# Kernel tuning notes

Hardware: AMD Instinct MI355X
Metric: run time of the kernel (lower is better)

Reference implementation:

```python
import jax, jax.numpy as jnp
import numpy as np

HEAD, D_MODEL, D_KV = 16, 1024, 64
B, NQ, NK = 2, 2048, 2048


def setup_inputs() -> dict:
    key = jax.random.key(0)
    ks = jax.random.split(key, 10)
    s = 1.0 / np.sqrt(D_MODEL)
    return {
        "queries": jax.random.normal(ks[0], (B, NQ, D_MODEL), jnp.float32),
        "keys": jax.random.normal(ks[1], (B, NK, D_MODEL), jnp.float32),
        "values": jax.random.normal(ks[2], (B, NK, D_MODEL), jnp.float32),
        "group_prob": jax.random.uniform(ks[3], (B, 1, NQ, NK), jnp.float32),
        "attention_mask": jnp.ones((B, NK), jnp.int32),
        "Wq": jax.random.normal(ks[4], (D_MODEL, HEAD * D_KV), jnp.float32) * s,
        "bq": jnp.zeros((HEAD * D_KV,), jnp.float32),
        "Wk": jax.random.normal(ks[5], (D_MODEL, HEAD * D_KV), jnp.float32) * s,
        "bk": jnp.zeros((HEAD * D_KV,), jnp.float32),
        "Wv": jax.random.normal(ks[6], (D_MODEL, HEAD * D_KV), jnp.float32) * s,
        "bv": jnp.zeros((HEAD * D_KV,), jnp.float32),
    }


def reference(queries, keys, values, group_prob, attention_mask, Wq, bq, Wk, bk, Wv, bv):
    b_s, nq, _ = queries.shape
    nk = keys.shape[1]
    # projections -> [b, h, n, d]
    q = (queries @ Wq + bq).reshape(b_s, nq, HEAD, D_KV).transpose(0, 2, 1, 3)
    k = (keys @ Wk + bk).reshape(b_s, nk, HEAD, D_KV).transpose(0, 2, 1, 3)
    v = (values @ Wv + bv).reshape(b_s, nk, HEAD, D_KV).transpose(0, 2, 1, 3)
    att = jnp.einsum("bhqd,bhkd->bhqk", q, k) / np.sqrt(D_KV).astype(np.float32)
    # NOTE: original uses non-in-place `att.masked_fill(...)` and discards the
    # result, so attention_mask has NO effect on the computation. Replicated.
    att = jax.nn.softmax(att, axis=-1)
    att = att * group_prob  # post-softmax group gating, broadcast over heads
    out = jnp.einsum("bhqk,bhkd->bhqd", att, v)
    return out.transpose(0, 2, 1, 3).reshape(b_s, nq, D_MODEL)
```

## Files before the change

kernel.cpp:

```cpp
#include <hip/hip_runtime.h>
#include <hip/hip_bf16.h>
#include <cstdint>

typedef unsigned short ushort_t;
typedef __attribute__((ext_vector_type(8))) short short8;
typedef __attribute__((ext_vector_type(4))) float floatx4;
typedef __attribute__((ext_vector_type(4))) unsigned short ushort4_t;

#define H_   16
#define DKV_ 64
#define DM_  1024
#define B_   2
#define NQ_  2048
#define NK_  2048

__device__ __forceinline__ unsigned short f2bf(float f) {
  union { float f; unsigned int u; } v; v.f = f;
  unsigned int u = v.u;
  return (unsigned short)((u + 0x7fffu + ((u >> 16) & 1u)) >> 16);
}

__device__ __forceinline__ float fexp2(float x) { return __builtin_amdgcn_exp2f(x); }
__device__ __forceinline__ float frcp(float x)  { return __builtin_amdgcn_rcpf(x); }

__device__ __forceinline__ floatx4 mfma16(short8 a, short8 b, floatx4 c) {
  return __builtin_amdgcn_mfma_f32_16x16x32_bf16(a, b, c, 0, 0, 0);
}

__device__ __forceinline__ void gload_lds16(const ushort_t* g, ushort_t* l) {
  __builtin_amdgcn_global_load_lds(
      (const __attribute__((address_space(1))) void*)g,
      (__attribute__((address_space(3))) void*)l, 16, 0, 0);
}

__global__ __launch_bounds__(256) void cast_x_kernel(
    const float* __restrict__ q, const float* __restrict__ k,
    const float* __restrict__ v, ushort_t* __restrict__ dst)
{
  const int t = blockIdx.y;
  const float* src = (t == 0) ? q : (t == 1) ? k : v;
  ushort_t* d = dst + (size_t)t * 4096 * 1024;
  const int gid = blockIdx.x * 256 + threadIdx.x;
  #pragma unroll
  for (int u = 0; u < 8; u++) {
    const int i4 = u * 131072 + gid;
    floatx4 f = ((const floatx4*)src)[i4];
    ushort4_t o;
    #pragma unroll
    for (int e = 0; e < 4; e++) o[e] = f2bf(f[e]);
    *(ushort4_t*)&d[(size_t)i4 * 4] = o;
  }
}

__global__ __launch_bounds__(256) void cast_wt_kernel(
    const float* __restrict__ Wq, const float* __restrict__ Wk,
    const float* __restrict__ Wv, ushort_t* __restrict__ WtAll)
{
  __shared__ ushort_t tile[32][33];
  const int t = blockIdx.z;
  const float* W = (t == 0) ? Wq : (t == 1) ? Wk : Wv;
  ushort_t* Wt = WtAll + (size_t)t * 1024 * 1024;
  const int n0 = blockIdx.x * 32, k0 = blockIdx.y * 32;
  const int tid = threadIdx.x, r = tid >> 3, c4 = (tid & 7) * 4;
  floatx4 f = *(const floatx4*)&W[(size_t)(k0 + r) * 1024 + n0 + c4];
  #pragma unroll
  for (int e = 0; e < 4; e++) tile[r][c4 + e] = f2bf(f[e]);
  __syncthreads();
  ushort4_t o;
  #pragma unroll
  for (int e = 0; e < 4; e++) o[e] = tile[c4 + e][r];
  *(ushort4_t*)&Wt[(size_t)(n0 + r) * 1024 + k0 + c4] = o;
}

__global__ __launch_bounds__(256, 2) void proj_kernel2(
    const ushort_t* __restrict__ Xbf, const ushort_t* __restrict__ WtAll,
    const float* __restrict__ bq, const float* __restrict__ bk,
    const float* __restrict__ bv,
    ushort_t* __restrict__ Qb, ushort_t* __restrict__ Kb, ushort_t* __restrict__ Vt)
{
  const int mode = blockIdx.z;
  const ushort_t* X  = Xbf  + (size_t)mode * 4096 * 1024;
  const ushort_t* Wt = WtAll + (size_t)mode * 1024 * 1024;
  const float* bias  = (mode == 0) ? bq : (mode == 1) ? bk : bv;
  ushort_t* dst      = (mode == 0) ? Qb : (mode == 1) ? Kb : Vt;

  __shared__ ushort_t SM[16384];

  const int tid = threadIdx.x, lane = tid & 63, wid = tid >> 6;
  const int c = lane & 15, g = lane >> 4;
  const int m0 = blockIdx.y * 128, n0 = blockIdx.x * 128;
  const int wm = wid & 1, wn = wid >> 1, mb = wm * 64, nb = wn * 64;
  const int srow = lane >> 2;
  const int schunk = (lane & 3) * 8;

  floatx4 acc[4][4];
  #pragma unroll
  for (int i = 0; i < 4; i++)
    #pragma unroll
    for (int j = 0; j < 4; j++) acc[i][j] = floatx4{0.f, 0.f, 0.f, 0.f};

  #pragma unroll
  for (int u = 0; u < 2; u++) {
    const int t = wid * 2 + u;
    gload_lds16(&X [(size_t)(m0 + t * 16 + srow) * 1024 + schunk], &SM[t * 512]);
    gload_lds16(&Wt[(size_t)(n0 + t * 16 + srow) * 1024 + schunk], &SM[4096 + t * 512]);
  }
  __syncthreads();

  for (int step = 0; step < 32; step++) {
    const int cur = step & 1, nxt = cur ^ 1;
    if (step + 1 < 32) {
      const int k1 = (step + 1) * 32;
      #pragma unroll
      for (int u = 0; u < 2; u++) {
        const int t = wid * 2 + u;
        gload_lds16(&X [(size_t)(m0 + t * 16 + srow) * 1024 + k1 + schunk],
                    &SM[nxt * 8192 + t * 512]);
        gload_lds16(&Wt[(size_t)(n0 + t * 16 + srow) * 1024 + k1 + schunk],
                    &SM[nxt * 8192 + 4096 + t * 512]);
      }
    }
    const ushort_t* SA = &SM[cur * 8192];
    const ushort_t* SB = &SM[cur * 8192 + 4096];
    short8 af[4], bfr[4];
    #pragma unroll
    for (int i = 0; i < 4; i++) af[i]  = *(const short8*)&SA[(mb + i * 16 + c) * 32 + g * 8];
    #pragma unroll
    for (int j = 0; j < 4; j++) bfr[j] = *(const short8*)&SB[(nb + j * 16 + c) * 32 + g * 8];
    #pragma unroll
    for (int i = 0; i < 4; i++)
      #pragma unroll
      for (int j = 0; j < 4; j++) acc[i][j] = mfma16(af[i], bfr[j], acc[i][j]);
    __syncthreads();
  }

  const float scale = (mode == 0) ? 0.18033688011112042f : 1.0f;
  ushort_t* EP = SM + wid * 2048;
  const int hh = (n0 + nb) >> 6;

  if (mode != 2) {
    for (int jj = 0; jj < 2; jj++) {
      #pragma unroll
      for (int jt = 0; jt < 2; jt++) {
        const int j = jj * 2 + jt;
        const float bb = bias[n0 + nb + j * 16 + c];
        #pragma unroll
        for (int i = 0; i < 4; i++)
          #pragma unroll
          for (int r = 0; r < 4; r++)
            EP[(i * 16 + g * 4 + r) * 32 + jt * 16 + c] =
                f2bf((acc[i][j][r] + bb) * scale);
      }
      #pragma unroll
      for (int u = 0; u < 8; u++) {
        const int rowl = u * 8 + (lane >> 3);
        ushort4_t vv = *(ushort4_t*)&EP[rowl * 32 + (lane & 7) * 4];
        const int rowg = m0 + mb + rowl;
        const int bb2 = rowg >> 11, nn = rowg & 2047;
        *(ushort4_t*)&dst[((size_t)(bb2 * H_ + hh) * NQ_ + nn) * DKV_ +
                          jj * 32 + (lane & 7) * 4] = vv;
      }
    }
  } else {
    const int bb2 = (m0 + mb) >> 11, nloc = (m0 + mb) & 2047;
    for (int j = 0; j < 4; j++) {
      const float bb = bias[n0 + nb + j * 16 + c];
      #pragma unroll
      for (int i = 0; i < 4; i++) {
        ushort4_t pk;
        #pragma unroll
        for (int r = 0; r < 4; r++) pk[r] = f2bf(acc[i][j][r] + bb);
        *(ushort4_t*)&EP[c * 72 + i * 16 + g * 4] = pk;
      }
      const int d0 = j * 16;
      #pragma unroll
      for (int u = 0; u < 2; u++) {
        const int coll = u * 8 + (lane >> 3);
        short8 vv = *(const short8*)&EP[coll * 72 + (lane & 7) * 8];
        *(short8*)&dst[((size_t)(bb2 * H_ + hh) * DKV_ + d0 + coll) * NK_ +
                       nloc + (lane & 7) * 8] = vv;
      }
    }
  }
}

constexpr int LDT = 40;
__global__ __launch_bounds__(256, 2) void proj_kernel_fb(
    const float* __restrict__ Xq, const float* __restrict__ Xk, const float* __restrict__ Xv,
    const float* __restrict__ Wq, const float* __restrict__ Wk, const float* __restrict__ Wv,
    const float* __restrict__ bq, const float* __restrict__ bk, const float* __restrict__ bv,
    ushort_t* __restrict__ Qb, ushort_t* __restrict__ Kb, ushort_t* __restrict__ Vt)
{
  const int mode = blockIdx.z;
  const float* X    = (mode == 0) ? Xq : (mode == 1) ? Xk : Xv;
  const float* W    = (mode == 0) ? Wq : (mode == 1) ? Wk : Wv;
  const float* bias = (mode == 0) ? bq : (mode == 1) ? bk : bv;
  ushort_t* dst     = (mode == 0) ? Qb : (mode == 1) ? Kb : Vt;

  __shared__ ushort_t Asm[128 * LDT];
  __shared__ ushort_t Bsm[128 * LDT];

  const int tid = threadIdx.x, lane = tid & 63, wid = tid >> 6;
  const int m0 = blockIdx.y * 128, n0 = blockIdx.x * 128;
  const int c = lane & 15, g = lane >> 4;
  const int wm = wid & 1, wn = wid >> 1, mb = wm * 64, nb = wn * 64;

  floatx4 acc[4][4];
  #pragma unroll
  for (int i = 0; i < 4; i++)
    #pragma unroll
    for (int j = 0; j < 4; j++) acc[i][j] = floatx4{0.f, 0.f, 0.f, 0.f};

  const int ar = tid >> 1, ah = tid & 1;
  const int bn = tid & 127, bh2 = tid >> 7;

  for (int k0 = 0; k0 < DM_; k0 += 32) {
    const floatx4* ap = (const floatx4*)(X + (size_t)(m0 + ar) * DM_ + k0 + ah * 16);
    floatx4 av0 = ap[0], av1 = ap[1], av2 = ap[2], av3 = ap[3];
    const float* wp = W + (size_t)(k0 + bh2 * 16) * 1024 + n0 + bn;
    float wv[16];
    #pragma unroll
    for (int j = 0; j < 16; j++) wv[j] = wp[j * 1024];
    short8 pa0, pa1, pb0, pb1;
    #pragma unroll
    for (int j = 0; j < 4; j++) {
      pa0[j] = (short)f2bf(av0[j]); pa0[4 + j] = (short)f2bf(av1[j]);
      pa1[j] = (short)f2bf(av2[j]); pa1[4 + j] = (short)f2bf(av3[j]);
    }
    #pragma unroll
    for (int j = 0; j < 8; j++) { pb0[j] = (short)f2bf(wv[j]); pb1[j] = (short)f2bf(wv[8 + j]); }
    __syncthreads();
    *(short8*)&Asm[ar * LDT + ah * 16]      = pa0;
    *(short8*)&Asm[ar * LDT + ah * 16 + 8]  = pa1;
    *(short8*)&Bsm[bn * LDT + bh2 * 16]     = pb0;
    *(short8*)&Bsm[bn * LDT + bh2 * 16 + 8] = pb1;
    __syncthreads();
    short8 af[4], bfr[4];
    #pragma unroll
    for (int i = 0; i < 4; i++) af[i]  = *(const short8*)&Asm[(mb + i * 16 + c) * LDT + g * 8];
    #pragma unroll
    for (int j = 0; j < 4; j++) bfr[j] = *(const short8*)&Bsm[(nb + j * 16 + c) * LDT + g * 8];
    #pragma unroll
    for (int i = 0; i < 4; i++)
      #pragma unroll
      for (int j = 0; j < 4; j++) acc[i][j] = mfma16(af[i], bfr[j], acc[i][j]);
  }
  #pragma unroll
  for (int j = 0; j < 4; j++) {
    const int col = n0 + nb + j * 16 + c;
    const float bv_ = bias[col];
    const int h = col >> 6, d = col & 63;
    #pragma unroll
    for (int i = 0; i < 4; i++)
      #pragma unroll
      for (int r = 0; r < 4; r++) {
        const int row = m0 + mb + i * 16 + g * 4 + r;
        const int b = row >> 11, n = row & 2047;
        float v = acc[i][j][r] + bv_;
        if (mode == 0) {
          v *= 0.18033688011112042f;
          dst[((size_t)(b * H_ + h) * NQ_ + n) * DKV_ + d] = f2bf(v);
        } else if (mode == 1) {
          dst[((size_t)(b * H_ + h) * NQ_ + n) * DKV_ + d] = f2bf(v);
        } else {
          dst[((size_t)(b * H_ + h) * DKV_ + d) * NK_ + n] = f2bf(v);
        }
      }
  }
}

__global__ __launch_bounds__(512, 4) void attn_kernel(
    const ushort_t* __restrict__ Qb, const ushort_t* __restrict__ Kb,
    const ushort_t* __restrict__ Vt, const float* __restrict__ gp,
    float* __restrict__ out)
{
  __shared__ ushort_t Ks[2][64 * 72];
  __shared__ ushort_t Vs[2][64 * 72];
  __shared__ ushort_t Pl[8][16 * 72];

  const int tid = threadIdx.x, lane = tid & 63, wid = tid >> 6;
  const int c = lane & 15, g = lane >> 4;
  const int h = blockIdx.x, b = blockIdx.z;
  const int bh = b * H_ + h;
  const int qw = blockIdx.y * 128 + wid * 16;

  const ushort_t* Qp = Qb + (size_t)bh * NQ_ * DKV_;
  const ushort_t* Kp = Kb + (size_t)bh * NK_ * DKV_;
  const ushort_t* Vp = Vt + (size_t)bh * DKV_ * NK_;
  const float* gpp = gp + (size_t)b * NQ_ * NK_ + (size_t)qw * NK_;
  ushort_t* Pw = Pl[wid];

  const int gx16 = (g >> 1) << 4;
  const int prd  = g ^ (((c >> 3) & 1) << 1);

  const int srow = tid >> 3;
  const int scol = (tid & 7) * 8;

  short8 qf[2];
  #pragma unroll
  for (int kc = 0; kc < 2; kc++)
    qf[kc] = *(const short8*)&Qp[(qw + c) * DKV_ + kc * 32 + g * 8];

  *(short8*)&Ks[0][srow * 72 + scol] = *(const short8*)&Kp[(size_t)srow * DKV_ + scol];
  *(short8*)&Vs[0][srow * 72 + scol] = *(const short8*)&Vp[(size_t)srow * NK_ + scol];
  __syncthreads();

  floatx4 o[4];
  float l[4];
  #pragma unroll
  for (int jd = 0; jd < 4; jd++) o[jd] = floatx4{0.f, 0.f, 0.f, 0.f};
  #pragma unroll
  for (int r = 0; r < 4; r++) l[r] = 0.f;

  for (int t = 0; t < NK_ / 64; t++) {
    const int k0 = t * 64;
    const int cur = t & 1, nxt = cur ^ 1;

    float gpv[4][4];
    #pragma unroll
    for (int r = 0; r < 4; r++) {
      const float* gq = gpp + (size_t)(g * 4 + r) * NK_ + k0 + c;
      #pragma unroll
      for (int jk = 0; jk < 4; jk++) gpv[jk][r] = gq[jk * 16];
    }

    short8 knx, vnx;
    const bool has_next = (t + 1) < NK_ / 64;
    if (has_next) {
      const int k1 = k0 + 64;
      knx = *(const short8*)&Kp[(size_t)(k1 + srow) * DKV_ + scol];
      vnx = *(const short8*)&Vp[(size_t)srow * NK_ + k1 + scol];
    }

    floatx4 s[4];
    #pragma unroll
    for (int jk = 0; jk < 4; jk++) s[jk] = floatx4{0.f, 0.f, 0.f, 0.f};
    #pragma unroll
    for (int jk = 0; jk < 4; jk++)
      #pragma unroll
      for (int kc = 0; kc < 2; kc++) {
        short8 kf = *(const short8*)&Ks[cur][(jk * 16 + c) * 72 + kc * 32 + g * 8];
        s[jk] = mfma16(qf[kc], kf, s[jk]);
      }

    #pragma unroll
    for (int jk = 0; jk < 4; jk++) {
      const int colw = (jk << 4) ^ gx16;
      #pragma unroll
      for (int r = 0; r < 4; r++) {
        const float p = fexp2(s[jk][r]);
        l[r] += p;
        Pw[(g * 4 + r) * 72 + colw + c] = f2bf(p * gpv[jk][r]);
      }
    }

    #pragma unroll
    for (int kc = 0; kc < 2; kc++) {
      short8 af = *(const short8*)&Pw[c * 72 + kc * 32 + prd * 8];
      #pragma unroll
      for (int jd = 0; jd < 4; jd++) {
        short8 vf = *(const short8*)&Vs[cur][(jd * 16 + c) * 72 + kc * 32 + g * 8];
        o[jd] = mfma16(af, vf, o[jd]);
      }
    }

    if (has_next) {
      *(short8*)&Ks[nxt][srow * 72 + scol] = knx;
      *(short8*)&Vs[nxt][srow * 72 + scol] = vnx;
    }
    __syncthreads();
  }

  float invl[4];
  #pragma unroll
  for (int r = 0; r < 4; r++) {
    float rs = l[r];
    rs += __shfl_xor(rs, 1);
    rs += __shfl_xor(rs, 2);
    rs += __shfl_xor(rs, 4);
    rs += __shfl_xor(rs, 8);
    invl[r] = frcp(rs);
  }
  #pragma unroll
  for (int jd = 0; jd < 4; jd++)
    #pragma unroll
    for (int r = 0; r < 4; r++) {
      const int row = qw + g * 4 + r;
      out[(size_t)(b * NQ_ + row) * 1024 + h * 64 + jd * 16 + c] =
          o[jd][r] * invl[r];
    }
}

extern "C" void kernel_launch(void* const* d_in, const int* in_sizes, int n_in,
                              void* d_out, int out_size, void* d_ws, size_t ws_size,
                              hipStream_t stream) {
  const float* queries = (const float*)d_in[0];
  const float* keys    = (const float*)d_in[1];
  const float* values  = (const float*)d_in[2];
  const float* gp      = (const float*)d_in[3];
  const float* Wq = (const float*)d_in[5];
  const float* bq = (const float*)d_in[6];
  const float* Wk = (const float*)d_in[7];
  const float* bk = (const float*)d_in[8];
  const float* Wv = (const float*)d_in[9];
  const float* bv = (const float*)d_in[10];

  const size_t SZ_QKV = (size_t)3 * B_ * H_ * NQ_ * DKV_;
  const size_t SZ_X   = (size_t)3 * 4096 * 1024;
  const size_t SZ_W   = (size_t)3 * 1024 * 1024;
  const size_t NEED   = (SZ_QKV + SZ_X + SZ_W) * sizeof(ushort_t);

  ushort_t* Qb = (ushort_t*)d_ws;
  ushort_t* Kb = Qb + (size_t)B_ * H_ * NQ_ * DKV_;
  ushort_t* Vt = Kb + (size_t)B_ * H_ * NK_ * DKV_;
  float* out = (float*)d_out;

  if (ws_size >= NEED) {
    ushort_t* Xbf = Qb + SZ_QKV;
    ushort_t* Wt  = Xbf + SZ_X;
    cast_x_kernel<<<dim3(512, 3), 256, 0, stream>>>(queries, keys, values, Xbf);
    cast_wt_kernel<<<dim3(32, 32, 3), 256, 0, stream>>>(Wq, Wk, Wv, Wt);
    proj_kernel2<<<dim3(8, 32, 3), 256, 0, stream>>>(
        Xbf, Wt, bq, bk, bv, Qb, Kb, Vt);
  } else {
    proj_kernel_fb<<<dim3(8, 32, 3), 256, 0, stream>>>(
        queries, keys, values, Wq, Wk, Wv, bq, bk, bv, Qb, Kb, Vt);
  }
  attn_kernel<<<dim3(H_, NQ_ / 128, B_), 512, 0, stream>>>(Qb, Kb, Vt, gp, out);
}
```

Measured before the change: 245.4 us.

## Prefetch group_prob one tile ahead and unroll attention loop by two

Loads the group_prob values for the next key tile one iteration ahead into ping-pong register arrays, so the global fp32 gating loads are hidden behind the current tile's MFMA work instead of stalling at the start of each iteration. The loop is manually unrolled by two so buffer indices are compile-time constants. The __syncthreads is replaced with an explicit lgkmcnt wait, s_barrier and sched_barrier. This adds register pressure (32 extra floats) under a 512-thread, 4-block launch bound, which could cause spills or lower occupancy.

```diff
diff --git a/kernel.cpp b/kernel.cpp
--- a/kernel.cpp
+++ b/kernel.cpp
@@ -31,6 +31,12 @@
   __builtin_amdgcn_global_load_lds(
       (const __attribute__((address_space(1))) void*)g,
       (__attribute__((address_space(3))) void*)l, 16, 0, 0);
+}
+
+__device__ __forceinline__ void block_sync_lds() {
+  asm volatile("s_waitcnt lgkmcnt(0)" ::: "memory");
+  __builtin_amdgcn_s_barrier();
+  __builtin_amdgcn_sched_barrier(0);
 }
 
 __global__ __launch_bounds__(256) void cast_x_kernel(
@@ -278,6 +284,8 @@
   __shared__ ushort_t Vs[2][64 * 72];
   __shared__ ushort_t Pl[8][16 * 72];
 
+  constexpr int NT = NK_ / 64;
+
   const int tid = threadIdx.x, lane = tid & 63, wid = tid >> 6;
   const int c = lane & 15, g = lane >> 4;
   const int h = blockIdx.x, b = blockIdx.z;
@@ -303,6 +311,13 @@
 
   *(short8*)&Ks[0][srow * 72 + scol] = *(const short8*)&Kp[(size_t)srow * DKV_ + scol];
   *(short8*)&Vs[0][srow * 72 + scol] = *(const short8*)&Vp[(size_t)srow * NK_ + scol];
+  float gpA[4][4], gpB[4][4];
+  #pragma unroll
+  for (int r = 0; r < 4; r++) {
+    const float* gq = gpp + (size_t)(g * 4 + r) * NK_ + c;
+    #pragma unroll
+    for (int jk = 0; jk < 4; jk++) gpA[jk][r] = gq[jk * 16];
+  }
   __syncthreads();
 
   floatx4 o[4];
@@ -312,64 +327,73 @@
   #pragma unroll
   for (int r = 0; r < 4; r++) l[r] = 0.f;
 
-  for (int t = 0; t < NK_ / 64; t++) {
-    const int k0 = t * 64;
-    const int cur = t & 1, nxt = cur ^ 1;
-
-    float gpv[4][4];
-    #pragma unroll
-    for (int r = 0; r < 4; r++) {
-      const float* gq = gpp + (size_t)(g * 4 + r) * NK_ + k0 + c;
-      #pragma unroll
-      for (int jk = 0; jk < 4; jk++) gpv[jk][r] = gq[jk * 16];
-    }
-
-    short8 knx, vnx;
-    const bool has_next = (t + 1) < NK_ / 64;
-    if (has_next) {
-      const int k1 = k0 + 64;
-      knx = *(const short8*)&Kp[(size_t)(k1 + srow) * DKV_ + scol];
-      vnx = *(const short8*)&Vp[(size_t)srow * NK_ + k1 + scol];
-    }
-
-    floatx4 s[4];
-    #pragma unroll
-    for (int jk = 0; jk < 4; jk++) s[jk] = floatx4{0.f, 0.f, 0.f, 0.f};
-    #pragma unroll
-    for (int jk = 0; jk < 4; jk++)
-      #pragma unroll
-      for (int kc = 0; kc < 2; kc++) {
-        short8 kf = *(const short8*)&Ks[cur][(jk * 16 + c) * 72 + kc * 32 + g * 8];
-        s[jk] = mfma16(qf[kc], kf, s[jk]);
-      }
-
-    #pragma unroll
-    for (int jk = 0; jk < 4; jk++) {
-      const int colw = (jk << 4) ^ gx16;
-      #pragma unroll
-      for (int r = 0; r < 4; r++) {
-        const float p = fexp2(s[jk][r]);
-        l[r] += p;
-        Pw[(g * 4 + r) * 72 + colw + c] = f2bf(p * gpv[jk][r]);
-      }
-    }
-
-    #pragma unroll
-    for (int kc = 0; kc < 2; kc++) {
-      short8 af = *(const short8*)&Pw[c * 72 + kc * 32 + prd * 8];
-      #pragma unroll
-      for (int jd = 0; jd < 4; jd++) {
-        short8 vf = *(const short8*)&Vs[cur][(jd * 16 + c) * 72 + kc * 32 + g * 8];
-        o[jd] = mfma16(af, vf, o[jd]);
-      }
-    }
-
-    if (has_next) {
-      *(short8*)&Ks[nxt][srow * 72 + scol] = knx;
-      *(short8*)&Vs[nxt][srow * 72 + scol] = vnx;
-    }
-    __syncthreads();
-  }
+#define ATTN_BODY(T, CUR, GPC, GPN)                                          \
+  {                                                                          \
+    const int t_ = (T);                                                      \
+    const int k0 = t_ * 64;                                                  \
+    const bool hn = (t_ + 1) < NT;                                           \
+                        \
+    short8 knx, vnx;                                                         \
+    if (hn) {                                                                \
+      const int k1 = k0 + 64;                                                \
+      knx = *(const short8*)&Kp[(size_t)(k1 + srow) * DKV_ + scol];          \
+      vnx = *(const short8*)&Vp[(size_t)srow * NK_ + k1 + scol];             \
+    }                                                                        \
+       \
+    if (hn) {                                                                \
+      const int k1 = k0 + 64;                                                \
+      _Pragma("unroll")                                                      \
+      for (int r = 0; r < 4; r++) {                                          \
+        const float* gq = gpp + (size_t)(g * 4 + r) * NK_ + k1 + c;          \
+        _Pragma("unroll")                                                    \
+        for (int jk = 0; jk < 4; jk++) GPN[jk][r] = gq[jk * 16];             \
+      }                                                                      \
+    }                                                                        \
+                                    \
+    floatx4 s_[4];                                                           \
+    _Pragma("unroll")                                                        \
+    for (int jk = 0; jk < 4; jk++) s_[jk] = floatx4{0.f, 0.f, 0.f, 0.f};     \
+    _Pragma("unroll")                                                        \
+    for (int jk = 0; jk < 4; jk++)                                           \
+      _Pragma("unroll")                                                      \
+      for (int kc = 0; kc < 2; kc++) {                                       \
+        short8 kf = *(const short8*)&Ks[CUR][(jk * 16 + c) * 72 + kc * 32 + g * 8]; \
+        s_[jk] = mfma16(qf[kc], kf, s_[jk]);                                 \
+      }                                                                      \
+              \
+    _Pragma("unroll")                                                        \
+    for (int jk = 0; jk < 4; jk++) {                                         \
+      const int colw = (jk << 4) ^ gx16;                                     \
+      _Pragma("unroll")                                                      \
+      for (int r = 0; r < 4; r++) {                                          \
+        const float p = fexp2(s_[jk][r]);                                    \
+        l[r] += p;                                                           \
+        Pw[(g * 4 + r) * 72 + colw + c] = f2bf(p * GPC[jk][r]);              \
+      }                                                                      \
+    }                                                                        \
+                         \
+    _Pragma("unroll")                                                        \
+    for (int kc = 0; kc < 2; kc++) {                                         \
+      short8 af = *(const short8*)&Pw[c * 72 + kc * 32 + prd * 8];           \
+      _Pragma("unroll")                                                      \
+      for (int jd = 0; jd < 4; jd++) {                                       \
+        short8 vf = *(const short8*)&Vs[CUR][(jd * 16 + c) * 72 + kc * 32 + g * 8]; \
+        o[jd] = mfma16(af, vf, o[jd]);                                       \
+      }                                                                      \
+    }                                                                        \
+     \
+    if (hn) {                                                                \
+      *(short8*)&Ks[(CUR) ^ 1][srow * 72 + scol] = knx;                      \
+      *(short8*)&Vs[(CUR) ^ 1][srow * 72 + scol] = vnx;                      \
+    }                                                                        \
+    block_sync_lds();                                                        \
+  }
+
+  for (int tt = 0; tt < NT; tt += 2) {
+    ATTN_BODY(tt,     0, gpA, gpB)
+    ATTN_BODY(tt + 1, 1, gpB, gpA)
+  }
+#undef ATTN_BODY
 
   float invl[4];
   #pragma unroll
```

After: 244.4 us. No clear change (-0.4%).
